# Optimization experiments

Measured on AMD Instinct MI355X. Metric: run time of the kernel, lower is better.

## Reference

```python
import jax, jax.numpy as jnp
import numpy as np

NUM_LAYERS = 2

def setup_inputs() -> dict:
    key = jax.random.key(0)
    ks = jax.random.split(key, 10)
    N, E, V, D, G = 50000, 800000, 100000, 128, 64
    node_ids = jax.random.randint(ks[0], (N,), 0, V)
    edge_index = jax.random.randint(ks[1], (2, E), 0, N)
    batch = jnp.sort(jax.random.randint(ks[2], (N,), 0, G))
    embed = jax.random.normal(ks[3], (V, D), dtype=jnp.float32)
    conv_w = jax.random.normal(ks[4], (NUM_LAYERS, D, D), dtype=jnp.float32) * (1.0 / np.sqrt(D))
    w_ih = jax.random.normal(ks[5], (3 * D, D), dtype=jnp.float32) * (1.0 / np.sqrt(D))
    w_hh = jax.random.normal(ks[6], (3 * D, D), dtype=jnp.float32) * (1.0 / np.sqrt(D))
    b_ih = jax.random.normal(ks[7], (3 * D,), dtype=jnp.float32) * 0.01
    b_hh = jax.random.normal(ks[8], (3 * D,), dtype=jnp.float32) * 0.01
    return {"node_ids": node_ids, "edge_index": edge_index, "batch": batch,
            "num_graphs": 64, "embed": embed, "conv_w": conv_w,
            "w_ih": w_ih, "w_hh": w_hh, "b_ih": b_ih, "b_hh": b_hh}


def _gru_cell(x, h, w_ih, w_hh, b_ih, b_hh):
    # torch.nn.GRUCell math; gate order r, z, n
    gi = x @ w_ih.T + b_ih
    gh = h @ w_hh.T + b_hh
    i_r, i_z, i_n = jnp.split(gi, 3, axis=-1)
    h_r, h_z, h_n = jnp.split(gh, 3, axis=-1)
    r = jax.nn.sigmoid(i_r + h_r)
    z = jax.nn.sigmoid(i_z + h_z)
    n = jnp.tanh(i_n + r * h_n)
    return (1.0 - z) * n + z * h


def reference(node_ids, edge_index, batch, num_graphs, embed, conv_w, w_ih, w_hh, b_ih, b_hh):
    N = node_ids.shape[0]
    src, dst = edge_index[0], edge_index[1]
    h = embed[node_ids]  # [N, D]
    for i in range(NUM_LAYERS):
        m = h @ conv_w[i]                                   # [N, D]
        agg = jax.ops.segment_sum(m[src], dst, num_segments=N)  # scatter-add messages
        h = _gru_cell(agg, h, w_ih, w_hh, b_ih, b_hh)
    # global mean pool per graph
    sums = jax.ops.segment_sum(h, batch, num_segments=num_graphs)       # [G, D]
    counts = jax.ops.segment_sum(jnp.ones((N,), h.dtype), batch, num_segments=num_graphs)
    return sums / jnp.maximum(counts, 1.0)[:, None]
```

## Files before the change

kernel.cpp:

```cpp
#include <hip/hip_runtime.h>
#include <hip/hip_bf16.h>


#define DTHREADS 256
#define BSHIFT 7
#define BNODES 128
#define BCAP 4096

typedef __attribute__((ext_vector_type(8))) short bf16x8;
typedef __attribute__((ext_vector_type(4))) float f32x4;

__device__ __forceinline__ float sigf(float x) { return 1.0f / (1.0f + __expf(-x)); }
__device__ __forceinline__ float tanhfast(float x) { return 1.0f - 2.0f / (1.0f + __expf(2.0f * x)); }

__device__ __forceinline__ unsigned short f2bf_rne(float x) {
  unsigned int u = __float_as_uint(x);
  u += 0x7fff + ((u >> 16) & 1);
  return (unsigned short)(u >> 16);
}
__device__ __forceinline__ float bf2f(unsigned int lo16) {
  return __uint_as_float(lo16 << 16);
}

__global__ __launch_bounds__(DTHREADS) void gather_kernel(
    const float* __restrict__ embed, const int* __restrict__ node_ids,
    unsigned short* __restrict__ hb, int N) {
  int idx = blockIdx.x * DTHREADS + threadIdx.x;
  if (idx >= N * 32) return;
  int n = idx >> 5;
  int c = (idx & 31) * 4;
  int v = node_ids[n];
  float4 val = *(const float4*)&embed[(size_t)v * 128 + c];
  unsigned short b[4] = {f2bf_rne(val.x), f2bf_rne(val.y), f2bf_rne(val.z), f2bf_rne(val.w)};
  *(ushort4*)&hb[(size_t)n * 128 + c] = *(ushort4*)b;
}

__global__ __launch_bounds__(DTHREADS) void pack_all_kernel(
    const float* __restrict__ w_hh, const float* __restrict__ conv_w,
    const float* __restrict__ w_ih, unsigned short* __restrict__ wpk_hh,
    unsigned short* __restrict__ wpk_wc, int nl,
    int* __restrict__ cur, int NB, float* __restrict__ outsum, int osz) {
  int id = blockIdx.x * DTHREADS + threadIdx.x;
  if (id < NB) cur[id] = 0;
  if (id < osz) outsum[id] = 0.f;
  int seg = id / (384 * 128);
  if (seg > nl) return;
  int r = id - seg * (384 * 128);
  int f = r >> 3, i = r & 7;
  int l = f & 63;
  int s = (f >> 6) & 3;
  int t = (f >> 8) & 3;
  int jb = f >> 10;
  int j = jb * 64 + t * 16 + (l & 15);
  int k = s * 32 + (l >> 4) * 8 + i;
  float val;
  unsigned short* dst;
  if (seg == 0) {
    val = w_hh[j * 128 + k];
    dst = wpk_hh;
  } else {
    const float* conv = conv_w + (size_t)(seg - 1) * 128 * 128;
    float acc = 0.f;
    for (int d = 0; d < 128; d += 4) {
      float4 cv = *(const float4*)&conv[k * 128 + d];
      float4 wv = *(const float4*)&w_ih[j * 128 + d];
      acc += cv.x * wv.x + cv.y * wv.y + cv.z * wv.z + cv.w * wv.w;
    }
    val = acc;
    dst = wpk_wc + (size_t)(seg - 1) * 384 * 128;
  }
  dst[(size_t)f * 8 + i] = f2bf_rne(val);
}

__global__ __launch_bounds__(DTHREADS) void bucket_scatter_kernel(
    const int* __restrict__ src, const int* __restrict__ dst,
    int* __restrict__ cur, unsigned int* __restrict__ ebuf, int E, int NB) {
  __shared__ int lc[512];
  __shared__ int lbs[512];
  int tid = threadIdx.x;
  for (int i = tid; i < NB; i += DTHREADS) lc[i] = 0;
  __syncthreads();
  int base = blockIdx.x * 4096;
  int rank[16];
  #pragma unroll
  for (int q = 0; q < 16; ++q) {
    int e = base + q * 256 + tid;
    if (e < E) rank[q] = atomicAdd(&lc[dst[e] >> BSHIFT], 1);
  }
  __syncthreads();
  for (int i = tid; i < NB; i += DTHREADS) {
    int c = lc[i];
    lbs[i] = c ? atomicAdd(&cur[i], c) : 0;
  }
  __syncthreads();
  #pragma unroll
  for (int q = 0; q < 16; ++q) {
    int e = base + q * 256 + tid;
    if (e < E) {
      int d = dst[e];
      int b = d >> BSHIFT;
      int slot = lbs[b] + rank[q];
      if (slot < BCAP)
        ebuf[(size_t)b * BCAP + slot] =
            (unsigned int)src[e] | ((unsigned int)(d & (BNODES - 1)) << 17);
    }
  }
}

__global__ __launch_bounds__(DTHREADS) void bucket_sort_kernel(
    const unsigned int* __restrict__ ebuf, const int* __restrict__ cur,
    int* __restrict__ row_start, int* __restrict__ row_end,
    int* __restrict__ csr_src, int N) {
  __shared__ int cnt[BNODES];
  __shared__ int sc[BNODES];
  const int tid = threadIdx.x;
  const int b = blockIdx.x;
  const int count = min(cur[b], BCAP);
  const unsigned int* eb = ebuf + (size_t)b * BCAP;
  int* cs = csr_src + (size_t)b * BCAP;
  if (tid < BNODES) cnt[tid] = 0;
  __syncthreads();
  for (int i = tid; i < count; i += DTHREADS)
    atomicAdd(&cnt[eb[i] >> 17], 1);
  __syncthreads();
  if (tid < BNODES) sc[tid] = cnt[tid];
  __syncthreads();
  #pragma unroll
  for (int off = 1; off < BNODES; off <<= 1) {
    int t = 0;
    if (tid < BNODES && tid >= off) t = sc[tid - off];
    __syncthreads();
    if (tid < BNODES) sc[tid] += t;
    __syncthreads();
  }
  if (tid < BNODES) {
    int excl = sc[tid] - cnt[tid];
    int n = b * BNODES + tid;
    if (n < N) {
      row_start[n] = b * BCAP + excl;
      row_end[n] = b * BCAP + sc[tid];
    }
    cnt[tid] = excl;
  }
  __syncthreads();
  for (int i = tid; i < count; i += DTHREADS) {
    unsigned int pk = eb[i];
    int slot = atomicAdd(&cnt[pk >> 17], 1);
    cs[slot] = (int)(pk & 0x1FFFFu);
  }
}

__global__ __launch_bounds__(512, 2) void fused_layer_kernel(
    const unsigned short* __restrict__ hold_buf,
    const int* __restrict__ row_start, const int* __restrict__ row_end,
    const int* __restrict__ csr_src,
    const unsigned short* __restrict__ wpk_wc, const unsigned short* __restrict__ wpk_hh,
    const float* __restrict__ b_ih, const float* __restrict__ b_hh,
    unsigned short* __restrict__ hnew_buf, int N, int nchunks) {
  __shared__ __align__(16) unsigned short Ag[32 * 128];
  __shared__ __align__(16) unsigned short Hs[32 * 128];
  const int tid = threadIdx.x;
  const int wv = tid >> 6, lane = tid & 63;
  const int lm = lane & 15, quad = lane >> 4;

  bf16x8 BI[3][4], BH[3][4];
  #pragma unroll
  for (int g = 0; g < 3; ++g) {
    int jb = g * 2 + (wv >> 2);
    int t = wv & 3;
    #pragma unroll
    for (int s = 0; s < 4; ++s) {
      size_t f = ((size_t)(jb * 4 + t) * 4 + s) * 64 + lane;
      BI[g][s] = *(const bf16x8*)&wpk_wc[f * 8];
      BH[g][s] = *(const bf16x8*)&wpk_hh[f * 8];
    }
  }

  const int jc = wv * 16 + lm;
  const float bir = b_ih[jc], biz = b_ih[128 + jc], bin_ = b_ih[256 + jc];
  const float bhr = b_hh[jc], bhz = b_hh[128 + jc], bhn = b_hh[256 + jc];
  const int c0 = jc >> 3, ej = jc & 7;

  const int srow = tid >> 4, scol = tid & 15;
  const int sdc = (scol ^ (srow & 15)) * 8;

  for (int ci = blockIdx.x; ci < nchunks; ci += gridDim.x) {
    int n = ci * 32 + srow;
    uint4 va = make_uint4(0, 0, 0, 0), vh = make_uint4(0, 0, 0, 0);
    if (n < N) {
      int s = row_start[n], e = row_end[n];
      float acc[8] = {0.f, 0.f, 0.f, 0.f, 0.f, 0.f, 0.f, 0.f};
      for (int i = s; i < e; i += 8) {
        int idx[8];
        #pragma unroll
        for (int q = 0; q < 8; ++q) {
          int ii = i + q;
          idx[q] = csr_src[ii < e ? ii : s];
        }
        uint4 d[8];
        #pragma unroll
        for (int q = 0; q < 8; ++q)
          d[q] = *(const uint4*)&hold_buf[(size_t)idx[q] * 128 + scol * 8];
        #pragma unroll
        for (int q = 0; q < 8; ++q) {
          if (i + q < e) {
            const unsigned int* dp = (const unsigned int*)&d[q];
            #pragma unroll
            for (int u = 0; u < 4; ++u) {
              acc[2 * u]     += bf2f(dp[u] & 0xffffu);
              acc[2 * u + 1] += bf2f(dp[u] >> 16);
            }
          }
        }
      }
      unsigned int o[4];
      #pragma unroll
      for (int q = 0; q < 4; ++q)
        o[q] = (unsigned int)f2bf_rne(acc[2 * q]) | ((unsigned int)f2bf_rne(acc[2 * q + 1]) << 16);
      va = *(uint4*)o;
      vh = *(const uint4*)&hold_buf[(size_t)n * 128 + scol * 8];
    }

    *(uint4*)&Ag[srow * 128 + sdc] = va;
    *(uint4*)&Hs[srow * 128 + sdc] = vh;
    __syncthreads();

    f32x4 accI[2][3], accH[2][3];
    #pragma unroll
    for (int mi = 0; mi < 2; ++mi)
      #pragma unroll
      for (int g = 0; g < 3; ++g) {
        accI[mi][g] = (f32x4){0.f, 0.f, 0.f, 0.f};
        accH[mi][g] = (f32x4){0.f, 0.f, 0.f, 0.f};
      }

    #pragma unroll
    for (int s = 0; s < 4; ++s) {
      bf16x8 afA[2], afH[2];
      #pragma unroll
      for (int mi = 0; mi < 2; ++mi) {
        int m = mi * 16 + lm;
        int chunk = (s * 4 + quad) ^ (m & 15);
        afA[mi] = *(const bf16x8*)&Ag[m * 128 + chunk * 8];
        afH[mi] = *(const bf16x8*)&Hs[m * 128 + chunk * 8];
      }
      #pragma unroll
      for (int g = 0; g < 3; ++g)
        #pragma unroll
        for (int mi = 0; mi < 2; ++mi) {
          accI[mi][g] = __builtin_amdgcn_mfma_f32_16x16x32_bf16(afA[mi], BI[g][s], accI[mi][g], 0, 0, 0);
          accH[mi][g] = __builtin_amdgcn_mfma_f32_16x16x32_bf16(afH[mi], BH[g][s], accH[mi][g], 0, 0, 0);
        }
    }

    const int n0 = ci * 32;
    #pragma unroll
    for (int mi = 0; mi < 2; ++mi) {
      #pragma unroll
      for (int r = 0; r < 4; ++r) {
        int row = mi * 16 + quad * 4 + r;
        int nn = n0 + row;
        if (nn >= N) continue;
        float ir = accI[mi][0][r] + bir;
        float iz = accI[mi][1][r] + biz;
        float in_ = accI[mi][2][r] + bin_;
        float hr = accH[mi][0][r] + bhr;
        float hz = accH[mi][1][r] + bhz;
        float hn = accH[mi][2][r] + bhn;
        float rr = sigf(ir + hr);
        float zz = sigf(iz + hz);
        float nn_ = tanhfast(in_ + rr * hn);
        float hold = bf2f((unsigned int)Hs[row * 128 + ((c0 ^ (row & 15)) * 8) + ej]);
        hnew_buf[(size_t)nn * 128 + jc] = f2bf_rne((1.f - zz) * nn_ + zz * hold);
      }
    }
    __syncthreads();
  }
}

__global__ __launch_bounds__(DTHREADS) void pool1_kernel(
    const unsigned short* __restrict__ hb, const int* __restrict__ batch,
    float* __restrict__ outsum, int N) {
  int b = blockIdx.x;
  int c = threadIdx.x & 127;
  int half = threadIdx.x >> 7;
  int nbeg = b * 64;
  int nend = min(nbeg + 64, N);
  float acc = 0.f;
  int cur = -1;
  for (int n = nbeg + half; n < nend; n += 2) {
    int g = batch[n];
    if (g != cur) {
      if (cur >= 0) atomicAdd(&outsum[(size_t)cur * 128 + c], acc);
      acc = 0.f;
      cur = g;
    }
    acc += bf2f((unsigned int)hb[(size_t)n * 128 + c]);
  }
  if (cur >= 0) atomicAdd(&outsum[(size_t)cur * 128 + c], acc);
}

__device__ __forceinline__ int lbound(const int* a, int n, int key) {
  int lo = 0, hi = n;
  while (lo < hi) {
    int mid = (lo + hi) >> 1;
    if (a[mid] < key) lo = mid + 1; else hi = mid;
  }
  return lo;
}

__global__ __launch_bounds__(128) void pool2_kernel(
    const float* __restrict__ outsum, const int* __restrict__ batch,
    float* __restrict__ out, int N) {
  int g = blockIdx.x;
  int c = threadIdx.x;
  int lo = lbound(batch, N, g);
  int hi = lbound(batch, N, g + 1);
  out[(size_t)g * 128 + c] = outsum[(size_t)g * 128 + c] / (float)max(hi - lo, 1);
}

extern "C" void kernel_launch(void* const* d_in, const int* in_sizes, int n_in,
                              void* d_out, int out_size, void* d_ws, size_t ws_size,
                              hipStream_t stream) {
  const int* node_ids = (const int*)d_in[0];
  const int* edge_index = (const int*)d_in[1];
  const int* batch = (const int*)d_in[2];
  const float* embed = (const float*)d_in[4];
  const float* conv_w = (const float*)d_in[5];
  const float* w_ih = (const float*)d_in[6];
  const float* w_hh = (const float*)d_in[7];
  const float* b_ih = (const float*)d_in[8];
  const float* b_hh = (const float*)d_in[9];
  float* out = (float*)d_out;

  const int N = in_sizes[0];
  const int E = in_sizes[1] / 2;
  const int G = out_size / 128;
  const int NUM_LAYERS = in_sizes[5] / (128 * 128);
  const int NB = (N + BNODES - 1) >> BSHIFT;

  const int* e_src = edge_index;
  const int* e_dst = edge_index + E;

  char* p = (char*)d_ws;
  unsigned short* hb = (unsigned short*)p;    p += (size_t)N * 128 * 2;
  unsigned short* h2 = (unsigned short*)p;    p += (size_t)N * 128 * 2;
  float* outsum = (float*)p;                  p += (size_t)G * 128 * 4;
  unsigned short* wpk_hh = (unsigned short*)p; p += (size_t)384 * 128 * 2;
  unsigned short* wpk_wc = (unsigned short*)p; p += (size_t)NUM_LAYERS * 384 * 128 * 2;
  int* cur = (int*)p;        p += 512 * 4;
  int* row_start = (int*)p;  p += (size_t)N * 4;
  int* row_end = (int*)p;    p += (size_t)N * 4;
  unsigned int* ebuf = (unsigned int*)p;  p += (size_t)NB * BCAP * 4;
  int* csr_src = (int*)p;    p += (size_t)NB * BCAP * 4;

  const int nEB = (E + 4095) / 4096;

  {
    int total = (NUM_LAYERS + 1) * 384 * 128;
    pack_all_kernel<<<(total + DTHREADS - 1) / DTHREADS, DTHREADS, 0, stream>>>(
        w_hh, conv_w, w_ih, wpk_hh, wpk_wc, NUM_LAYERS, cur, NB, outsum, G * 128);
  }

  bucket_scatter_kernel<<<nEB, DTHREADS, 0, stream>>>(e_src, e_dst, cur, ebuf, E, NB);
  bucket_sort_kernel<<<NB, DTHREADS, 0, stream>>>(ebuf, cur, row_start, row_end, csr_src, N);

  gather_kernel<<<(N * 32 + DTHREADS - 1) / DTHREADS, DTHREADS, 0, stream>>>(embed, node_ids, hb, N);

  const int nchunks = (N + 31) / 32;
  for (int L = 0; L < NUM_LAYERS; ++L) {
    const unsigned short* ho = (L & 1) ? h2 : hb;
    unsigned short* hn = (L & 1) ? hb : h2;
    fused_layer_kernel<<<512, 512, 0, stream>>>(
        ho, row_start, row_end, csr_src, wpk_wc + (size_t)L * 384 * 128,
        wpk_hh, b_ih, b_hh, hn, N, nchunks);
  }
  const unsigned short* hfin = (NUM_LAYERS & 1) ? h2 : hb;

  const int pblocks = (N + 63) / 64;
  pool1_kernel<<<pblocks, DTHREADS, 0, stream>>>(hfin, batch, outsum, N);
  pool2_kernel<<<G, 128, 0, stream>>>(outsum, batch, out, N);
}
```

Before: 310.6 us.

## Balance edge aggregation across rows with edge-split partitioning and LDS atomics

Instead of one 16-thread group handling each node's whole edge list, the chunk's 32-node edge range is split evenly across the 32 row groups. Each group walks a contiguous edge slice, keeps a running sum per destination row, and flushes it to a shared fp32 accumulator with LDS atomicAdd when the row changes. The CSR array now stores the packed local destination index alongside the source so the row can be recovered. This targets load imbalance from skewed degrees, at the cost of an extra 16KB of LDS, two more barriers per chunk, and LDS atomics. It also fetches 4 edges per iteration instead of 8, leaving fewer gathers in flight.

```diff
diff --git a/kernel.cpp b/kernel.cpp
--- a/kernel.cpp
+++ b/kernel.cpp
@@ -110,14 +110,14 @@
 __global__ __launch_bounds__(DTHREADS) void bucket_sort_kernel(
     const unsigned int* __restrict__ ebuf, const int* __restrict__ cur,
     int* __restrict__ row_start, int* __restrict__ row_end,
-    int* __restrict__ csr_src, int N) {
+    int* __restrict__ csr_pk, int N) {
   __shared__ int cnt[BNODES];
   __shared__ int sc[BNODES];
   const int tid = threadIdx.x;
   const int b = blockIdx.x;
   const int count = min(cur[b], BCAP);
   const unsigned int* eb = ebuf + (size_t)b * BCAP;
-  int* cs = csr_src + (size_t)b * BCAP;
+  int* cs = csr_pk + (size_t)b * BCAP;
   if (tid < BNODES) cnt[tid] = 0;
   __syncthreads();
   for (int i = tid; i < count; i += DTHREADS)
@@ -146,17 +146,18 @@
   for (int i = tid; i < count; i += DTHREADS) {
     unsigned int pk = eb[i];
     int slot = atomicAdd(&cnt[pk >> 17], 1);
-    cs[slot] = (int)(pk & 0x1FFFFu);
+    cs[slot] = (int)pk;
   }
 }
 
 __global__ __launch_bounds__(512, 2) void fused_layer_kernel(
     const unsigned short* __restrict__ hold_buf,
     const int* __restrict__ row_start, const int* __restrict__ row_end,
-    const int* __restrict__ csr_src,
+    const int* __restrict__ csr_pk,
     const unsigned short* __restrict__ wpk_wc, const unsigned short* __restrict__ wpk_hh,
     const float* __restrict__ b_ih, const float* __restrict__ b_hh,
     unsigned short* __restrict__ hnew_buf, int N, int nchunks) {
+  __shared__ __align__(16) float Ac[32 * 128];
   __shared__ __align__(16) unsigned short Ag[32 * 128];
   __shared__ __align__(16) unsigned short Hs[32 * 128];
   const int tid = threadIdx.x;
@@ -185,44 +186,85 @@
   const int sdc = (scol ^ (srow & 15)) * 8;
 
   for (int ci = blockIdx.x; ci < nchunks; ci += gridDim.x) {
-    int n = ci * 32 + srow;
-    uint4 va = make_uint4(0, 0, 0, 0), vh = make_uint4(0, 0, 0, 0);
-    if (n < N) {
-      int s = row_start[n], e = row_end[n];
-      float acc[8] = {0.f, 0.f, 0.f, 0.f, 0.f, 0.f, 0.f, 0.f};
-      for (int i = s; i < e; i += 8) {
-        int idx[8];
+    const int n0 = ci * 32;
+
+    {
+      int n = n0 + srow;
+      uint4 vh = make_uint4(0, 0, 0, 0);
+      if (n < N) vh = *(const uint4*)&hold_buf[(size_t)n * 128 + scol * 8];
+      *(uint4*)&Hs[srow * 128 + sdc] = vh;
+      f32x4 z = {0.f, 0.f, 0.f, 0.f};
+      *(f32x4*)&Ac[srow * 128 + scol * 8] = z;
+      *(f32x4*)&Ac[srow * 128 + scol * 8 + 4] = z;
+    }
+    __syncthreads();
+
+    {
+      const int co = n0 & 127;
+      const int lastn = min(n0 + 31, N - 1);
+      const int S = row_start[n0];
+      const int E = row_end[lastn];
+      const int L = (E - S + 31) >> 5;
+      int gb = S + srow * L;
+      int ge = min(gb + L, E);
+      float a[8] = {0.f, 0.f, 0.f, 0.f, 0.f, 0.f, 0.f, 0.f};
+      int curRow = -1;
+      for (int i = gb; i < ge; i += 4) {
+        unsigned int pk[4];
+        uint4 d[4];
         #pragma unroll
-        for (int q = 0; q < 8; ++q) {
-          int ii = i + q;
-          idx[q] = csr_src[ii < e ? ii : s];
+        for (int q = 0; q < 4; ++q) {
+          int e = (i + q < ge) ? i + q : i;
+          pk[q] = (unsigned int)csr_pk[e];
         }
-        uint4 d[8];
         #pragma unroll
-        for (int q = 0; q < 8; ++q)
-          d[q] = *(const uint4*)&hold_buf[(size_t)idx[q] * 128 + scol * 8];
+        for (int q = 0; q < 4; ++q)
+          d[q] = *(const uint4*)&hold_buf[(size_t)(pk[q] & 0x1FFFFu) * 128 + scol * 8];
         #pragma unroll
-        for (int q = 0; q < 8; ++q) {
-          if (i + q < e) {
+        for (int q = 0; q < 4; ++q) {
+          if (i + q < ge) {
+            int row = (int)((pk[q] >> 17) & 127u) - co;
+            if (row != curRow) {
+              if (curRow >= 0) {
+                #pragma unroll
+                for (int u = 0; u < 8; ++u) {
+                  int w = (u + scol + curRow) & 7;
+                  atomicAdd(&Ac[curRow * 128 + scol * 8 + w], a[w]);
+                }
+              }
+              #pragma unroll
+              for (int u = 0; u < 8; ++u) a[u] = 0.f;
+              curRow = row;
+            }
             const unsigned int* dp = (const unsigned int*)&d[q];
             #pragma unroll
             for (int u = 0; u < 4; ++u) {
-              acc[2 * u]     += bf2f(dp[u] & 0xffffu);
-              acc[2 * u + 1] += bf2f(dp[u] >> 16);
+              a[2 * u]     += bf2f(dp[u] & 0xffffu);
+              a[2 * u + 1] += bf2f(dp[u] >> 16);
             }
           }
         }
       }
+      if (curRow >= 0) {
+        #pragma unroll
+        for (int u = 0; u < 8; ++u) {
+          int w = (u + scol + curRow) & 7;
+          atomicAdd(&Ac[curRow * 128 + scol * 8 + w], a[w]);
+        }
+      }
+    }
+    __syncthreads();
+
+    {
       unsigned int o[4];
       #pragma unroll
-      for (int q = 0; q < 4; ++q)
-        o[q] = (unsigned int)f2bf_rne(acc[2 * q]) | ((unsigned int)f2bf_rne(acc[2 * q + 1]) << 16);
-      va = *(uint4*)o;
-      vh = *(const uint4*)&hold_buf[(size_t)n * 128 + scol * 8];
-    }
-
-    *(uint4*)&Ag[srow * 128 + sdc] = va;
-    *(uint4*)&Hs[srow * 128 + sdc] = vh;
+      for (int q = 0; q < 4; ++q) {
+        float x0 = Ac[srow * 128 + scol * 8 + 2 * q];
+        float x1 = Ac[srow * 128 + scol * 8 + 2 * q + 1];
+        o[q] = (unsigned int)f2bf_rne(x0) | ((unsigned int)f2bf_rne(x1) << 16);
+      }
+      *(uint4*)&Ag[srow * 128 + sdc] = *(uint4*)o;
+    }
     __syncthreads();
 
     f32x4 accI[2][3], accH[2][3];
@@ -253,7 +295,6 @@
         }
     }
 
-    const int n0 = ci * 32;
     #pragma unroll
     for (int mi = 0; mi < 2; ++mi) {
       #pragma unroll
@@ -352,7 +393,7 @@
   int* row_start = (int*)p;  p += (size_t)N * 4;
   int* row_end = (int*)p;    p += (size_t)N * 4;
   unsigned int* ebuf = (unsigned int*)p;  p += (size_t)NB * BCAP * 4;
-  int* csr_src = (int*)p;    p += (size_t)NB * BCAP * 4;
+  int* csr_pk = (int*)p;     p += (size_t)NB * BCAP * 4;
 
   const int nEB = (E + 4095) / 4096;
 
@@ -363,7 +404,7 @@
   }
 
   bucket_scatter_kernel<<<nEB, DTHREADS, 0, stream>>>(e_src, e_dst, cur, ebuf, E, NB);
-  bucket_sort_kernel<<<NB, DTHREADS, 0, stream>>>(ebuf, cur, row_start, row_end, csr_src, N);
+  bucket_sort_kernel<<<NB, DTHREADS, 0, stream>>>(ebuf, cur, row_start, row_end, csr_pk, N);
 
   gather_kernel<<<(N * 32 + DTHREADS - 1) / DTHREADS, DTHREADS, 0, stream>>>(embed, node_ids, hb, N);
 
@@ -372,7 +413,7 @@
     const unsigned short* ho = (L & 1) ? h2 : hb;
     unsigned short* hn = (L & 1) ? hb : h2;
     fused_layer_kernel<<<512, 512, 0, stream>>>(
-        ho, row_start, row_end, csr_src, wpk_wc + (size_t)L * 384 * 128,
+        ho, row_start, row_end, csr_pk, wpk_wc + (size_t)L * 384 * 128,
         wpk_hh, b_ih, b_hh, hn, N, nchunks);
   }
   const unsigned short* hfin = (NUM_LAYERS & 1) ? h2 : hb;
```

New measurement: 395.0 us. 27.2% more time.
